# Kernel optimization log

Hardware: AMD Instinct MI355X
Metric: run time of the kernel (lower is better)

Reference implementation:

```python
import jax, jax.numpy as jnp
import numpy as np

N_NODES = 100_000
N_EDGES = 1_600_000
IN_DIM, HIDDEN, Z_DIM = 64, 128, 64


def _gcn_conv(x, src, dst, dinv, W, b, n):
    # PyG GCNConv: out_i = sum_j (d_i^-1/2 d_j^-1/2) (x_j @ W) + b, edges incl. self-loops
    xw = x @ W                                   # [N, out]
    norm = dinv[src] * dinv[dst]                 # [E+N]
    msg = xw[src] * norm[:, None]                # [E+N, out]
    return jax.ops.segment_sum(msg, dst, num_segments=n) + b


def _prep_graph(edge_index, n):
    loop = jnp.arange(n, dtype=edge_index.dtype)
    src = jnp.concatenate([edge_index[0], loop])
    dst = jnp.concatenate([edge_index[1], loop])
    deg = jax.ops.segment_sum(jnp.ones_like(dst, dtype=jnp.float32), dst, num_segments=n)
    dinv = jnp.where(deg > 0, jax.lax.rsqrt(jnp.maximum(deg, 1.0)), 0.0)
    return src, dst, dinv


def setup_inputs() -> dict:
    key = jax.random.key(0)
    ks = jax.random.split(key, 8)
    x = jax.random.normal(ks[0], (N_NODES, IN_DIM), dtype=jnp.float32)
    edge_index = jax.random.randint(ks[1], (2, N_EDGES), 0, N_NODES, dtype=jnp.int32)

    def glorot(k, fi, fo):
        s = (6.0 / (fi + fo)) ** 0.5
        return jax.random.uniform(k, (fi, fo), jnp.float32, -s, s)

    return {
        "x": x, "edge_index": edge_index,
        "W1": glorot(ks[2], IN_DIM, HIDDEN), "b1": jnp.zeros((HIDDEN,), jnp.float32),
        "W2": glorot(ks[3], HIDDEN, HIDDEN), "b2": jnp.zeros((HIDDEN,), jnp.float32),
        "Wmu": glorot(ks[4], HIDDEN, Z_DIM), "bmu": jnp.zeros((Z_DIM,), jnp.float32),
        "Wlv": glorot(ks[5], HIDDEN, Z_DIM), "blv": jnp.zeros((Z_DIM,), jnp.float32),
    }


def reference(x, edge_index, W1, b1, W2, b2, Wmu, bmu, Wlv, blv):
    n = x.shape[0]
    src, dst, dinv = _prep_graph(edge_index, n)
    h = jax.nn.relu(_gcn_conv(x, src, dst, dinv, W1, b1, n))
    h = jax.nn.relu(_gcn_conv(h, src, dst, dinv, W2, b2, n))
    # dropout p=0.0 (eval): identity
    mu = _gcn_conv(h, src, dst, dinv, Wmu, bmu, n)
    logvar = _gcn_conv(h, src, dst, dinv, Wlv, blv, n)
    return (mu, logvar)
```

## Files before the change

kernel.cpp:

```cpp
#include <hip/hip_runtime.h>
#include <hip/hip_fp16.h>
#include <cstddef>

#define N_NODES 100000
#define N_EDGES 1600000
#define E_TOT   (N_EDGES + N_NODES)
#define IN_DIM  64
#define HIDDEN  128
#define Z_DIM   64

#define BN 128
#define NB ((N_NODES + BN - 1) / BN)
#define NBLK 256
#define GN  ((N_NODES + 255) / 256)

#define EM_CAP (E_TOT + 15 * N_NODES + 64)

using f16x8 = __attribute__((ext_vector_type(8))) _Float16;
using f32x4 = __attribute__((ext_vector_type(4))) float;


__global__ __launch_bounds__(256) void prep_k(const float* __restrict__ x, __half* __restrict__ x16,
                                              const float* __restrict__ W1, const float* __restrict__ W2,
                                              const float* __restrict__ Wmu, const float* __restrict__ Wlv,
                                              __half* __restrict__ W1t, __half* __restrict__ W2t,
                                              __half* __restrict__ Wht, int* __restrict__ cnt) {
    int i = blockIdx.x * 256 + threadIdx.x;
    const int CAST = N_NODES * IN_DIM / 8;
    if (i < CAST) {
        const float4* in4 = (const float4*)x;
        float4 a = in4[2 * i], b = in4[2 * i + 1];
        __half2 h0 = __floats2half2_rn(a.x, a.y);
        __half2 h1 = __floats2half2_rn(a.z, a.w);
        __half2 h2 = __floats2half2_rn(b.x, b.y);
        __half2 h3 = __floats2half2_rn(b.z, b.w);
        uint4 pk = make_uint4(*(unsigned*)&h0, *(unsigned*)&h1, *(unsigned*)&h2, *(unsigned*)&h3);
        ((uint4*)x16)[i] = pk;
        return;
    }
    int j = i - CAST;
    if (j < 128 * 64) {
        int col = j >> 6, k = j & 63;
        W1t[j] = __float2half(W1[k * 128 + col]);
        return;
    }
    int m = j - 128 * 64;
    if (m < 128 * 128) {
        int col = m >> 7, k = m & 127;
        W2t[m] = __float2half(W2[k * 128 + col]);
        return;
    }
    int h = m - 128 * 128;
    if (h < 128 * 128) {
        int col = h >> 7, k = h & 127;
        Wht[h] = __float2half(col < 64 ? Wmu[k * 64 + col] : Wlv[k * 64 + (col - 64)]);
        return;
    }
    int z = h - 128 * 128;
    if (z < N_NODES / 4) ((int4*)cnt)[z] = make_int4(0, 0, 0, 0);
}


__global__ __launch_bounds__(256) void count4_k(const int* __restrict__ dst, int* cnt, int e4) {
    int i = blockIdx.x * 256 + threadIdx.x;
    if (i < e4) {
        int4 d = ((const int4*)dst)[i];
        atomicAdd(&cnt[d.x], 1);
        atomicAdd(&cnt[d.y], 1);
        atomicAdd(&cnt[d.z], 1);
        atomicAdd(&cnt[d.w], 1);
    }
}

__global__ __launch_bounds__(256) void scan_block_k(const int* __restrict__ cnt, int* __restrict__ rowptr,
                                                    int2* __restrict__ bsum, int* __restrict__ rawAt,
                                                    float* __restrict__ dinv, int n) {
    __shared__ int sp[256], sr[256];
    int tid = threadIdx.x;
    int i = blockIdx.x * 256 + tid;
    int deg = (i < n) ? cnt[i] + 1 : 0;
    int pad = (deg + 15) & ~15;
    int raw = (i < n) ? deg - 1 : 0;
    if (i < n) dinv[i] = rsqrtf((float)deg);
    sp[tid] = pad; sr[tid] = raw;
    __syncthreads();
#pragma unroll
    for (int off = 1; off < 256; off <<= 1) {
        int t1 = (tid >= off) ? sp[tid - off] : 0;
        int t2 = (tid >= off) ? sr[tid - off] : 0;
        __syncthreads();
        sp[tid] += t1; sr[tid] += t2;
        __syncthreads();
    }
    if (i < n) rowptr[i] = sp[tid] - pad;
    if (i < n && tid == 0)   rawAt[i >> 7] = 0;
    if (i < n && tid == 128) rawAt[i >> 7] = sr[127];
    if (tid == 255) bsum[blockIdx.x] = make_int2(sp[255], sr[255]);
}

__global__ __launch_bounds__(512) void scan_addm_k(int* __restrict__ rowptr, const int2* __restrict__ bsum,
                                                   const int* __restrict__ rawAt, int* __restrict__ ebase,
                                                   int* __restrict__ bcur, int n, int e, int nb) {
    __shared__ int sp[512], sr[512];
    __shared__ int tot;
    int tid = threadIdx.x;
    int2 v = (tid < nb) ? bsum[tid] : make_int2(0, 0);
    sp[tid] = v.x; sr[tid] = v.y;
    __syncthreads();
#pragma unroll
    for (int off = 1; off < 512; off <<= 1) {
        int t1 = (tid >= off) ? sp[tid - off] : 0;
        int t2 = (tid >= off) ? sr[tid - off] : 0;
        __syncthreads();
        sp[tid] += t1; sr[tid] += t2;
        __syncthreads();
    }
    if (tid == 511) tot = sp[511];
    __syncthreads();
    sp[tid] -= v.x; sr[tid] -= v.y;
    __syncthreads();
    if (tid < 256) {
        int i = blockIdx.x * 256 + tid;
        if (i < n) {
            int val = rowptr[i] + sp[blockIdx.x];
            rowptr[i] = val;
            if ((i & 127) == 0) {
                int b = i >> 7;
                int eb = rawAt[b] + sr[b >> 1];
                ebase[b] = eb;
                bcur[b] = eb;
            }
        }
        if (i == 0) { rowptr[n] = tot; ebase[NB] = e; }
    }
}

__global__ __launch_bounds__(256) void binA_k(const int* __restrict__ src, const int* __restrict__ dst,
                                              int* __restrict__ bcur, int* __restrict__ binned, int e) {
    __shared__ int hist[NB];
    __shared__ int cur[NB];
    int t = threadIdx.x;
    int ch = (e + gridDim.x - 1) / gridDim.x;
    int i0 = blockIdx.x * ch;
    int i1 = i0 + ch; if (i1 > e) i1 = e;

    for (int b = t; b < NB; b += 256) hist[b] = 0;
    __syncthreads();
    for (int i = i0 + t; i < i1; i += 256)
        atomicAdd(&hist[dst[i] >> 7], 1);
    __syncthreads();
    for (int b = t; b < NB; b += 256) {
        int h = hist[b];
        cur[b] = h ? atomicAdd(&bcur[b], h) : 0;
    }
    __syncthreads();
    for (int i = i0 + t; i < i1; i += 256) {
        int s = src[i], d = dst[i];
        int p = atomicAdd(&cur[d >> 7], 1);
        binned[p] = ((d & 127) << 17) | s;
    }
}

__global__ __launch_bounds__(256) void place_k(const int* __restrict__ binned, const int* __restrict__ ebase,
                                               const int* __restrict__ rowptr, const float* __restrict__ dinv,
                                               int2* __restrict__ em, int n) {
    __shared__ int cur[BN];
    __shared__ float sdv[BN];
    int b = blockIdx.x, t = threadIdx.x;
    int n0 = b * BN;
    int nn = n - n0; if (nn > BN) nn = BN;
    if (t < nn) {
        int rp = rowptr[n0 + t];
        float dv = dinv[n0 + t];
        sdv[t] = dv;
        em[rp] = make_int2(n0 + t, __float_as_int(dv * dv));
        cur[t] = rp + 1;
    }
    __syncthreads();
    int e0 = ebase[b], e1 = ebase[b + 1];
    for (int i = e0 + t; i < e1; i += 256) {
        int pk = binned[i];
        int ld = pk >> 17, s = pk & 0x1FFFF;
        int q = atomicAdd(&cur[ld], 1);
        em[q] = make_int2(s, __float_as_int(dinv[s] * sdv[ld]));
    }
    __syncthreads();
    if (t < nn) {
        int pe = rowptr[n0 + t + 1];
        int node = n0 + t;
        for (int p = cur[t]; p < pe; p++) em[p] = make_int2(node, 0);
    }
}


template <int DIM, bool HEAD>
__global__ __launch_bounds__(256) void agg_k(const __half* __restrict__ H, const int* __restrict__ rowptr,
                                             const int2* __restrict__ em, __half* __restrict__ out,
                                             const float* __restrict__ bmu, const float* __restrict__ blv,
                                             float* __restrict__ mu, float* __restrict__ lv, int n) {
    int node = (int)((blockIdx.x * 256 + threadIdx.x) >> 6);
    if (node >= n) return;
    int lane = threadIdx.x & 63;
    int beg = rowptr[node], end = rowptr[node + 1];
    int lastIdx = rowptr[n] - 1;
    const uint4* H4 = (const uint4*)H;

    constexpr int RV   = DIM / 8;
    constexpr int SUBS = 64 / RV;
    constexpr int STEP = SUBS * 2;
    int sub = lane / RV;
    int fl  = lane % RV;

    float acc[8];
#pragma unroll
    for (int q = 0; q < 8; q++) acc[q] = 0.f;

    auto meta = [&](int j, int p, int& s, float& w) {
        int ci = j + SUBS * p + sub;
        ci = min(ci, lastIdx);
        int2 e = em[ci];
        s = e.x;
        w = __int_as_float(e.y);
    };
    auto rows = [&](int s0, int s1, uint4& r0, uint4& r1) {
        r0 = H4[(size_t)s0 * RV + fl];
        r1 = H4[(size_t)s1 * RV + fl];
    };
    auto fmas = [&](const uint4& r0, const uint4& r1, float ww0, float ww1) {
        const __half* h0 = (const __half*)&r0;
        const __half* h1 = (const __half*)&r1;
#pragma unroll
        for (int q = 0; q < 8; q++) acc[q] = fmaf(ww0, __half2float(h0[q]), acc[q]);
#pragma unroll
        for (int q = 0; q < 8; q++) acc[q] = fmaf(ww1, __half2float(h1[q]), acc[q]);
    };

    int G = (end - beg) / STEP;

    int   sa0, sa1, sb0, sb1, sc0, sc1, sd0, sd1;
    float wa0, wa1, wb0, wb1, wc0, wc1, wd0, wd1;
    uint4 ra0, ra1, rb0, rb1, rc0, rc1, rd0, rd1;

    meta(beg,            0, sa0, wa0); meta(beg,            1, sa1, wa1);
    meta(beg + STEP,     0, sb0, wb0); meta(beg + STEP,     1, sb1, wb1);
    rows(sa0, sa1, ra0, ra1);
    rows(sb0, sb1, rb0, rb1);
    meta(beg + 2 * STEP, 0, sc0, wc0); meta(beg + 2 * STEP, 1, sc1, wc1);
    meta(beg + 3 * STEP, 0, sd0, wd0); meta(beg + 3 * STEP, 1, sd1, wd1);

    int g = 0;
    int jf = beg + 4 * STEP;
    while (true) {
        rows(sc0, sc1, rc0, rc1);
        fmas(ra0, ra1, wa0, wa1);
        if (++g >= G) break;
        meta(jf, 0, sa0, wa0); meta(jf, 1, sa1, wa1); jf += STEP;

        rows(sd0, sd1, rd0, rd1);
        fmas(rb0, rb1, wb0, wb1);
        if (++g >= G) break;
        meta(jf, 0, sb0, wb0); meta(jf, 1, sb1, wb1); jf += STEP;

        rows(sa0, sa1, ra0, ra1);
        fmas(rc0, rc1, wc0, wc1);
        if (++g >= G) break;
        meta(jf, 0, sc0, wc0); meta(jf, 1, sc1, wc1); jf += STEP;

        rows(sb0, sb1, rb0, rb1);
        fmas(rd0, rd1, wd0, wd1);
        if (++g >= G) break;
        meta(jf, 0, sd0, wd0); meta(jf, 1, sd1, wd1); jf += STEP;
    }

#pragma unroll
    for (int off = 32; off >= RV; off >>= 1) {
#pragma unroll
        for (int q = 0; q < 8; q++) acc[q] += __shfl_xor(acc[q], off);
    }
    if (sub == 0) {
        if constexpr (HEAD) {
            const float* bp = (fl < 8) ? (bmu + fl * 8) : (blv + (fl - 8) * 8);
#pragma unroll
            for (int q = 0; q < 8; q++) acc[q] += bp[q];
            float* op = (fl < 8) ? (mu + (size_t)node * 64 + fl * 8)
                                 : (lv + (size_t)node * 64 + (fl - 8) * 8);
            *(float4*)op = make_float4(acc[0], acc[1], acc[2], acc[3]);
            *(float4*)(op + 4) = make_float4(acc[4], acc[5], acc[6], acc[7]);
        } else {
            __half2 q0 = __floats2half2_rn(acc[0], acc[1]);
            __half2 q1 = __floats2half2_rn(acc[2], acc[3]);
            __half2 q2 = __floats2half2_rn(acc[4], acc[5]);
            __half2 q3 = __floats2half2_rn(acc[6], acc[7]);
            uint4 pk = make_uint4(*(unsigned*)&q0, *(unsigned*)&q1, *(unsigned*)&q2, *(unsigned*)&q3);
            *(uint4*)(out + (size_t)node * DIM + fl * 8) = pk;
        }
    }
}


template <int K, bool BR>
__global__ __launch_bounds__(256) void mgemm_k(const __half* __restrict__ A,
                                               const __half* __restrict__ Wt,
                                               const float* __restrict__ bias,
                                               __half* __restrict__ C, int n) {
    __shared__ __align__(16) __half Wl[128 * K];
    int t = threadIdx.x;

    constexpr int CHUNKS = 128 * K / 8;
    const uint4* Wg = (const uint4*)Wt;
    for (int i = t; i < CHUNKS; i += 256) {
        int g = i * 16;
        int col = g / (2 * K);
        uint4 v = Wg[i];
        *(uint4*)((char*)Wl + (g ^ ((col & 7) << 4))) = v;
    }
    __syncthreads();

    int lane = t & 63, w = t >> 6;
    int colb = lane & 15;
    int kq = (lane >> 4) * 8;
    int m0 = blockIdx.x * 64 + w * 16;
    int rowA = m0 + colb; if (rowA >= n) rowA = n - 1;
    const __half* Arow = A + (size_t)rowA * K + kq;

    f32x4 acc[8];
#pragma unroll
    for (int c = 0; c < 8; c++) acc[c] = (f32x4){0.f, 0.f, 0.f, 0.f};

    const char* wb = (const char*)Wl;
    int swz = (colb & 7) << 4;
    int off0 = colb * (2 * K) + kq * 2;

#pragma unroll
    for (int k0 = 0; k0 < K; k0 += 32) {
        f16x8 a = *(const f16x8*)(Arow + k0);
#pragma unroll
        for (int c = 0; c < 8; c++) {
            f16x8 b = *(const f16x8*)(wb + ((off0 + c * (32 * K) + k0 * 2) ^ swz));
            acc[c] = __builtin_amdgcn_mfma_f32_16x16x32_f16(a, b, acc[c], 0, 0, 0);
        }
    }

    int rbase = m0 + (lane >> 4) * 4;
#pragma unroll
    for (int c = 0; c < 8; c++) {
        int col = c * 16 + colb;
        float bv = BR ? bias[col] : 0.f;
#pragma unroll
        for (int r = 0; r < 4; r++) {
            int row = rbase + r;
            if (row < n) {
                float v = acc[c][r] + bv;
                if (BR) v = fmaxf(v, 0.f);
                C[(size_t)row * 128 + col] = __float2half(v);
            }
        }
    }
}


extern "C" void kernel_launch(void* const* d_in, const int* in_sizes, int n_in,
                              void* d_out, int out_size, void* d_ws, size_t ws_size,
                              hipStream_t stream) {
    const int N = N_NODES, E = N_EDGES;

    const float* x    = (const float*)d_in[0];
    const int*   ei   = (const int*)d_in[1];
    const int*   srcA = ei;
    const int*   dstA = ei + E;
    const float* W1   = (const float*)d_in[2];
    const float* b1   = (const float*)d_in[3];
    const float* W2   = (const float*)d_in[4];
    const float* b2   = (const float*)d_in[5];
    const float* Wmu  = (const float*)d_in[6];
    const float* bmu  = (const float*)d_in[7];
    const float* Wlv  = (const float*)d_in[8];
    const float* blv  = (const float*)d_in[9];
    float* out = (float*)d_out;

    char* ws = (char*)d_ws;
    size_t o = 0;
    auto alloc = [&](size_t bytes) -> void* {
        o = (o + 255) & ~(size_t)255;
        void* p = ws + o;
        o += bytes;
        return p;
    };
    int*    cnt    = (int*)alloc((size_t)N * 4);
    int*    rowptr = (int*)alloc((size_t)(N + 1) * 4);
    float*  dinv   = (float*)alloc((size_t)N * 4);
    int2*   bsum   = (int2*)alloc(512 * 8);
    int*    rawAt  = (int*)alloc((size_t)NB * 4);
    int*    ebase  = (int*)alloc((size_t)(NB + 1) * 4);
    int*    bcur   = (int*)alloc((size_t)(NB + 1) * 4);
    int2*   em     = (int2*)alloc((size_t)EM_CAP * 8);
    int*    binned = (int*)alloc((size_t)E * 4);
    __half* x16    = (__half*)alloc((size_t)N * IN_DIM * 2);
    __half* B1     = (__half*)alloc((size_t)N * HIDDEN * 2);
    __half* B2     = (__half*)alloc((size_t)N * HIDDEN * 2);
    __half* W1t    = (__half*)alloc(128 * 64 * 2);
    __half* W2t    = (__half*)alloc(128 * 128 * 2);
    __half* Wht    = (__half*)alloc(128 * 128 * 2);
    (void)ws_size;

    const int PREP_T = N * IN_DIM / 8 + 128 * 64 + 128 * 128 + 128 * 128 + N / 4;
    const int gPrep = (PREP_T + 255) / 256;
    const int gC4  = (E / 4 + 255) / 256;
    const int gAgg = (N + 3) / 4;
    const int gMg  = (N + 63) / 64;

    prep_k<<<gPrep, 256, 0, stream>>>(x, x16, W1, W2, Wmu, Wlv, W1t, W2t, Wht, cnt);
    count4_k<<<gC4, 256, 0, stream>>>(dstA, cnt, E / 4);
    scan_block_k<<<GN, 256, 0, stream>>>(cnt, rowptr, bsum, rawAt, dinv, N);
    scan_addm_k<<<GN, 512, 0, stream>>>(rowptr, bsum, rawAt, ebase, bcur, N, E, GN);
    binA_k<<<NBLK, 256, 0, stream>>>(srcA, dstA, bcur, binned, E);
    place_k<<<NB, 256, 0, stream>>>(binned, ebase, rowptr, dinv, em, N);

    agg_k<64, false><<<gAgg, 256, 0, stream>>>(x16, rowptr, em, B1, nullptr, nullptr, nullptr, nullptr, N);
    mgemm_k<64, true><<<gMg, 256, 0, stream>>>(B1, W1t, b1, B2, N);

    agg_k<128, false><<<gAgg, 256, 0, stream>>>(B2, rowptr, em, B1, nullptr, nullptr, nullptr, nullptr, N);
    mgemm_k<128, true><<<gMg, 256, 0, stream>>>(B1, W2t, b2, B2, N);

    mgemm_k<128, false><<<gMg, 256, 0, stream>>>(B2, Wht, nullptr, B1, N);
    agg_k<128, true><<<gAgg, 256, 0, stream>>>(B1, rowptr, em, nullptr, bmu, blv,
                                               out, out + (size_t)N * Z_DIM, N);
}
```

Before: 425.7 us.

## Build CSR from bucket histogram, drop per-node degree scan and padding

After: 724.0 us. 70.1% more time.

```diff
diff --git a/kernel.cpp b/kernel.cpp
--- a/kernel.cpp
+++ b/kernel.cpp
@@ -12,9 +12,6 @@
 #define BN 128
 #define NB ((N_NODES + BN - 1) / BN)
 #define NBLK 256
-#define GN  ((N_NODES + 255) / 256)
-
-#define EM_CAP (E_TOT + 15 * N_NODES + 64)
 
 using f16x8 = __attribute__((ext_vector_type(8))) _Float16;
 using f32x4 = __attribute__((ext_vector_type(4))) float;
@@ -24,7 +21,8 @@
                                               const float* __restrict__ W1, const float* __restrict__ W2,
                                               const float* __restrict__ Wmu, const float* __restrict__ Wlv,
                                               __half* __restrict__ W1t, __half* __restrict__ W2t,
-                                              __half* __restrict__ Wht, int* __restrict__ cnt) {
+                                              __half* __restrict__ Wht,
+                                              const int* __restrict__ dst, int* __restrict__ bhist) {
     int i = blockIdx.x * 256 + threadIdx.x;
     const int CAST = N_NODES * IN_DIM / 8;
     if (i < CAST) {
@@ -57,82 +55,31 @@
         return;
     }
     int z = h - 128 * 128;
-    if (z < N_NODES / 4) ((int4*)cnt)[z] = make_int4(0, 0, 0, 0);
-}
-
-
-__global__ __launch_bounds__(256) void count4_k(const int* __restrict__ dst, int* cnt, int e4) {
-    int i = blockIdx.x * 256 + threadIdx.x;
-    if (i < e4) {
-        int4 d = ((const int4*)dst)[i];
-        atomicAdd(&cnt[d.x], 1);
-        atomicAdd(&cnt[d.y], 1);
-        atomicAdd(&cnt[d.z], 1);
-        atomicAdd(&cnt[d.w], 1);
-    }
-}
-
-__global__ __launch_bounds__(256) void scan_block_k(const int* __restrict__ cnt, int* __restrict__ rowptr,
-                                                    int2* __restrict__ bsum, int* __restrict__ rawAt,
-                                                    float* __restrict__ dinv, int n) {
-    __shared__ int sp[256], sr[256];
-    int tid = threadIdx.x;
-    int i = blockIdx.x * 256 + tid;
-    int deg = (i < n) ? cnt[i] + 1 : 0;
-    int pad = (deg + 15) & ~15;
-    int raw = (i < n) ? deg - 1 : 0;
-    if (i < n) dinv[i] = rsqrtf((float)deg);
-    sp[tid] = pad; sr[tid] = raw;
-    __syncthreads();
-#pragma unroll
-    for (int off = 1; off < 256; off <<= 1) {
-        int t1 = (tid >= off) ? sp[tid - off] : 0;
-        int t2 = (tid >= off) ? sr[tid - off] : 0;
+    if (z < N_EDGES / 4) {
+        int4 d = ((const int4*)dst)[z];
+        atomicAdd(&bhist[d.x >> 7], 1);
+        atomicAdd(&bhist[d.y >> 7], 1);
+        atomicAdd(&bhist[d.z >> 7], 1);
+        atomicAdd(&bhist[d.w >> 7], 1);
+    }
+}
+
+__global__ __launch_bounds__(1024) void bscan_k(const int* __restrict__ bhist, int* __restrict__ ebase,
+                                                int* __restrict__ bcur, int e) {
+    __shared__ int s[1024];
+    int t = threadIdx.x;
+    int v = (t < NB) ? bhist[t] : 0;
+    s[t] = v;
+    __syncthreads();
+#pragma unroll
+    for (int off = 1; off < 1024; off <<= 1) {
+        int x = (t >= off) ? s[t - off] : 0;
         __syncthreads();
-        sp[tid] += t1; sr[tid] += t2;
+        s[t] += x;
         __syncthreads();
     }
-    if (i < n) rowptr[i] = sp[tid] - pad;
-    if (i < n && tid == 0)   rawAt[i >> 7] = 0;
-    if (i < n && tid == 128) rawAt[i >> 7] = sr[127];
-    if (tid == 255) bsum[blockIdx.x] = make_int2(sp[255], sr[255]);
-}
-
-__global__ __launch_bounds__(512) void scan_addm_k(int* __restrict__ rowptr, const int2* __restrict__ bsum,
-                                                   const int* __restrict__ rawAt, int* __restrict__ ebase,
-                                                   int* __restrict__ bcur, int n, int e, int nb) {
-    __shared__ int sp[512], sr[512];
-    __shared__ int tot;
-    int tid = threadIdx.x;
-    int2 v = (tid < nb) ? bsum[tid] : make_int2(0, 0);
-    sp[tid] = v.x; sr[tid] = v.y;
-    __syncthreads();
-#pragma unroll
-    for (int off = 1; off < 512; off <<= 1) {
-        int t1 = (tid >= off) ? sp[tid - off] : 0;
-        int t2 = (tid >= off) ? sr[tid - off] : 0;
-        __syncthreads();
-        sp[tid] += t1; sr[tid] += t2;
-        __syncthreads();
-    }
-    if (tid == 511) tot = sp[511];
-    __syncthreads();
-    sp[tid] -= v.x; sr[tid] -= v.y;
-    __syncthreads();
-    if (tid < 256) {
-        int i = blockIdx.x * 256 + tid;
-        if (i < n) {
-            int val = rowptr[i] + sp[blockIdx.x];
-            rowptr[i] = val;
-            if ((i & 127) == 0) {
-                int b = i >> 7;
-                int eb = rawAt[b] + sr[b >> 1];
-                ebase[b] = eb;
-                bcur[b] = eb;
-            }
-        }
-        if (i == 0) { rowptr[n] = tot; ebase[NB] = e; }
-    }
+    if (t < NB) { int ex = s[t] - v; ebase[t] = ex; bcur[t] = ex; }
+    if (t == 0) ebase[NB] = e;
 }
 
 __global__ __launch_bounds__(256) void binA_k(const int* __restrict__ src, const int* __restrict__ dst,
@@ -161,7 +108,38 @@
     }
 }
 
-__global__ __launch_bounds__(256) void place_k(const int* __restrict__ binned, const int* __restrict__ ebase,
+__global__ __launch_bounds__(256) void pdeg_k(const int* __restrict__ binned, const int* __restrict__ ebase,
+                                              int* __restrict__ rowptr, float* __restrict__ dinv, int n) {
+    __shared__ int hist[BN];
+    __shared__ int sc[BN];
+    int b = blockIdx.x, t = threadIdx.x;
+    int n0 = b * BN;
+    int nn = n - n0; if (nn > BN) nn = BN;
+    if (t < BN) hist[t] = (t < nn) ? 1 : 0;
+    __syncthreads();
+    int e0 = ebase[b], e1 = ebase[b + 1];
+    for (int i = e0 + t; i < e1; i += 256)
+        atomicAdd(&hist[binned[i] >> 17], 1);
+    __syncthreads();
+    int v = (t < BN) ? hist[t] : 0;
+    if (t < BN) sc[t] = v;
+    __syncthreads();
+#pragma unroll
+    for (int off = 1; off < BN; off <<= 1) {
+        int x = (t < BN && t >= off) ? sc[t - off] : 0;
+        __syncthreads();
+        if (t < BN) sc[t] += x;
+        __syncthreads();
+    }
+    int base = e0 + n0;
+    if (t < nn) {
+        rowptr[n0 + t] = base + sc[t] - v;
+        dinv[n0 + t] = rsqrtf((float)v);
+    }
+    if (b == gridDim.x - 1 && t == 0) rowptr[n] = E_TOT;
+}
+
+__global__ __launch_bounds__(256) void pfill_k(const int* __restrict__ binned, const int* __restrict__ ebase,
                                                const int* __restrict__ rowptr, const float* __restrict__ dinv,
                                                int2* __restrict__ em, int n) {
     __shared__ int cur[BN];
@@ -184,12 +162,6 @@
         int q = atomicAdd(&cur[ld], 1);
         em[q] = make_int2(s, __float_as_int(dinv[s] * sdv[ld]));
     }
-    __syncthreads();
-    if (t < nn) {
-        int pe = rowptr[n0 + t + 1];
-        int node = n0 + t;
-        for (int p = cur[t]; p < pe; p++) em[p] = make_int2(node, 0);
-    }
 }
 
 
@@ -202,7 +174,6 @@
     if (node >= n) return;
     int lane = threadIdx.x & 63;
     int beg = rowptr[node], end = rowptr[node + 1];
-    int lastIdx = rowptr[n] - 1;
     const uint4* H4 = (const uint4*)H;
 
     constexpr int RV   = DIM / 8;
@@ -216,11 +187,11 @@
     for (int q = 0; q < 8; q++) acc[q] = 0.f;
 
     auto meta = [&](int j, int p, int& s, float& w) {
-        int ci = j + SUBS * p + sub;
-        ci = min(ci, lastIdx);
-        int2 e = em[ci];
+        int idx = j + SUBS * p + sub;
+        int ci  = idx < end ? idx : beg;
+        int2 e  = em[ci];
         s = e.x;
-        w = __int_as_float(e.y);
+        w = idx < end ? __int_as_float(e.y) : 0.f;
     };
     auto rows = [&](int s0, int s1, uint4& r0, uint4& r1) {
         r0 = H4[(size_t)s0 * RV + fl];
@@ -235,7 +206,7 @@
         for (int q = 0; q < 8; q++) acc[q] = fmaf(ww1, __half2float(h1[q]), acc[q]);
     };
 
-    int G = (end - beg) / STEP;
+    int G = (end - beg + STEP - 1) / STEP;
 
     int   sa0, sa1, sb0, sb1, sc0, sc1, sd0, sd1;
     float wa0, wa1, wb0, wb1, wc0, wc1, wd0, wd1;
@@ -362,7 +333,7 @@
 extern "C" void kernel_launch(void* const* d_in, const int* in_sizes, int n_in,
                               void* d_out, int out_size, void* d_ws, size_t ws_size,
                               hipStream_t stream) {
-    const int N = N_NODES, E = N_EDGES;
+    const int N = N_NODES, E = N_EDGES, ETOT = E_TOT;
 
     const float* x    = (const float*)d_in[0];
     const int*   ei   = (const int*)d_in[1];
@@ -386,14 +357,12 @@
         o += bytes;
         return p;
     };
-    int*    cnt    = (int*)alloc((size_t)N * 4);
+    int*    bhist  = (int*)alloc((size_t)(NB + 1) * 4);
+    int*    ebase  = (int*)alloc((size_t)(NB + 1) * 4);
+    int*    bcur   = (int*)alloc((size_t)(NB + 1) * 4);
     int*    rowptr = (int*)alloc((size_t)(N + 1) * 4);
     float*  dinv   = (float*)alloc((size_t)N * 4);
-    int2*   bsum   = (int2*)alloc(512 * 8);
-    int*    rawAt  = (int*)alloc((size_t)NB * 4);
-    int*    ebase  = (int*)alloc((size_t)(NB + 1) * 4);
-    int*    bcur   = (int*)alloc((size_t)(NB + 1) * 4);
-    int2*   em     = (int2*)alloc((size_t)EM_CAP * 8);
+    int2*   em     = (int2*)alloc((size_t)ETOT * 8);
     int*    binned = (int*)alloc((size_t)E * 4);
     __half* x16    = (__half*)alloc((size_t)N * IN_DIM * 2);
     __half* B1     = (__half*)alloc((size_t)N * HIDDEN * 2);
@@ -403,18 +372,17 @@
     __half* Wht    = (__half*)alloc(128 * 128 * 2);
     (void)ws_size;
 
-    const int PREP_T = N * IN_DIM / 8 + 128 * 64 + 128 * 128 + 128 * 128 + N / 4;
+    const int PREP_T = N * IN_DIM / 8 + 128 * 64 + 128 * 128 + 128 * 128 + E / 4;
     const int gPrep = (PREP_T + 255) / 256;
-    const int gC4  = (E / 4 + 255) / 256;
     const int gAgg = (N + 3) / 4;
     const int gMg  = (N + 63) / 64;
 
-    prep_k<<<gPrep, 256, 0, stream>>>(x, x16, W1, W2, Wmu, Wlv, W1t, W2t, Wht, cnt);
-    count4_k<<<gC4, 256, 0, stream>>>(dstA, cnt, E / 4);
-    scan_block_k<<<GN, 256, 0, stream>>>(cnt, rowptr, bsum, rawAt, dinv, N);
-    scan_addm_k<<<GN, 512, 0, stream>>>(rowptr, bsum, rawAt, ebase, bcur, N, E, GN);
+    hipMemsetAsync(bhist, 0, (size_t)NB * 4, stream);
+    prep_k<<<gPrep, 256, 0, stream>>>(x, x16, W1, W2, Wmu, Wlv, W1t, W2t, Wht, dstA, bhist);
+    bscan_k<<<1, 1024, 0, stream>>>(bhist, ebase, bcur, E);
     binA_k<<<NBLK, 256, 0, stream>>>(srcA, dstA, bcur, binned, E);
-    place_k<<<NB, 256, 0, stream>>>(binned, ebase, rowptr, dinv, em, N);
+    pdeg_k<<<NB, 256, 0, stream>>>(binned, ebase, rowptr, dinv, N);
+    pfill_k<<<NB, 256, 0, stream>>>(binned, ebase, rowptr, dinv, em, N);
 
     agg_k<64, false><<<gAgg, 256, 0, stream>>>(x16, rowptr, em, B1, nullptr, nullptr, nullptr, nullptr, N);
     mgemm_k<64, true><<<gMg, 256, 0, stream>>>(B1, W1t, b1, B2, N);
```
